# Kernel tuning notes

Hardware: AMD Instinct MI355X
Metric: run time of the kernel (lower is better)

## Reference

```python
import jax, jax.numpy as jnp
import numpy as np

B, S, E, FF = 8, 16384, 256, 1024
H, W, G = 128, 128, 16
Hn, Wn = H // G, W // G


def setup_inputs() -> dict:
    key = jax.random.key(0)
    ks = jax.random.split(key, 16)
    w = lambda k, shape: jax.random.normal(k, shape, jnp.float32) * 0.02
    return {
        "x": jax.random.normal(ks[0], (B, S, E), jnp.float32),
        "Wq": w(ks[1], (E, E)), "bq": jnp.zeros((E,), jnp.float32),
        "Wk": w(ks[2], (E, E)), "bk": jnp.zeros((E,), jnp.float32),
        "Wv": w(ks[3], (E, E)), "bv": jnp.zeros((E,), jnp.float32),
        "Wo": w(ks[4], (E, E)), "bo": jnp.zeros((E,), jnp.float32),
        "W1": w(ks[5], (E, FF)), "b1": jnp.zeros((FF,), jnp.float32),
        "W2": w(ks[6], (FF, E)), "b2": jnp.zeros((E,), jnp.float32),
        "g1": jnp.ones((E,), jnp.float32), "be1": jnp.zeros((E,), jnp.float32),
        "g2": jnp.ones((E,), jnp.float32), "be2": jnp.zeros((E,), jnp.float32),
    }


def _ln(x, g, b, eps=1e-5):
    m = jnp.mean(x, axis=-1, keepdims=True)
    v = jnp.mean(jnp.square(x - m), axis=-1, keepdims=True)
    return (x - m) * jax.lax.rsqrt(v + eps) * g + b


def _forward(x, Wq, bq, Wk, bk, Wv, bv, Wo, bo, W1, b1, W2, b2, g1, be1, g2, be2):
    # x: (B, S, E) -> (B, E, H, W), faithful to torch reshape (row-major reinterpret)
    x4 = x.reshape(B, E, H, W)
    # window partition: each window is the contiguous (E, G, G) block the torch loop slices
    xw = x4.reshape(B, E, Hn, G, Wn, G).transpose(0, 2, 4, 1, 3, 5)  # (B,Hn,Wn,E,G,G)
    # faithful raw reinterpretation (E,G,G) -> (G*G, E), matching grid.reshape(B,-1,E)
    t = xw.reshape(B, Hn * Wn, G * G, E)  # (B, nW, T=256, E)
    # single-head self-attention per window (batched over all windows at once)
    q = jnp.einsum('bwte,ef->bwtf', t, Wq) + bq
    k = jnp.einsum('bwte,ef->bwtf', t, Wk) + bk
    v = jnp.einsum('bwte,ef->bwtf', t, Wv) + bv
    scores = jnp.einsum('bwqe,bwke->bwqk', q, k) / jnp.sqrt(jnp.float32(E))
    attn = jax.nn.softmax(scores, axis=-1)
    o = jnp.einsum('bwqk,bwke->bwqe', attn, v)
    o = jnp.einsum('bwte,ef->bwtf', o, Wo) + bo  # (B, nW, 256, E)
    # reverse: view each window back to (E,G,G) and reassemble the feature map
    y = o.reshape(B, Hn, Wn, E, G, G).transpose(0, 3, 1, 4, 2, 5).reshape(B, E, H, W)
    y = y.reshape(B, S, E)  # faithful x.view(B, -1, E)
    # FFN (dropout is identity in eval) + residual with post-LN as written
    h = jax.nn.gelu(jnp.einsum('bse,ef->bsf', y, W1) + b1, approximate=False)
    ffn = jnp.einsum('bsf,fe->bse', h, W2) + b2
    y = y + _ln(ffn, g1, be1)
    y = y + _ln(y, g2, be2)
    return y


def reference(x, Wq, bq, Wk, bk, Wv, bv, Wo, bo, W1, b1, W2, b2, g1, be1, g2, be2):
    return _forward(x, Wq, bq, Wk, bk, Wv, bv, Wo, bo, W1, b1, W2, b2, g1, be1, g2, be2)
```

## Files before the change

### kernel.cpp

```cpp
#include <hip/hip_runtime.h>
#include <hip/hip_bf16.h>


typedef __bf16 bf16x8 __attribute__((ext_vector_type(8)));
typedef float  f32x4  __attribute__((ext_vector_type(4)));
typedef unsigned short us16;
typedef us16 us16x8 __attribute__((ext_vector_type(8)));
typedef us16 us16x4 __attribute__((ext_vector_type(4)));
typedef us16 us16x2 __attribute__((ext_vector_type(2)));

#define DI static __device__ __forceinline__

DI us16 f2b(float f){ __bf16 h = (__bf16)f; return __builtin_bit_cast(us16, h); }

DI bf16x8 cvt8(f32x4 a, f32x4 b){
  bf16x8 r;
  r[0]=(__bf16)a[0]; r[1]=(__bf16)a[1]; r[2]=(__bf16)a[2]; r[3]=(__bf16)a[3];
  r[4]=(__bf16)b[0]; r[5]=(__bf16)b[1]; r[6]=(__bf16)b[2]; r[7]=(__bf16)b[3];
  return r;
}
DI bf16x8 ld8(const us16* p){
  us16x8 v = *(const us16x8*)p;
  return __builtin_bit_cast(bf16x8, v);
}
DI f32x4 mfma16(bf16x8 a, bf16x8 b, f32x4 c){
  return __builtin_amdgcn_mfma_f32_16x16x32_bf16(a, b, c, 0, 0, 0);
}

DI bf16x8 ld_sw8(const char* base, int row, int f0){
  return ld8((const us16*)(base + row*512 + ((((f0>>3) ^ (row&7))) << 4)));
}
DI void st_sw1(char* base, int row, int f, us16 v){
  *(us16*)(base + row*512 + ((((f>>3) ^ (row&7))) << 4) + (f&7)*2) = v;
}
DI void st_sw4(char* base, int row, int f0, us16x4 v){
  *(us16x4*)(base + row*512 + ((((f0>>3) ^ (row&7))) << 4) + (f0&7)*2) = v;
}

DI bf16x8 ld_vt(const char* base, int row, int gg){
  return ld8((const us16*)(base + row*64 + (((gg ^ ((row>>1)&3))) << 4)));
}
DI void st_vt(char* base, int row, int col, us16 v){
  int c = col >> 3;
  *(us16*)(base + row*64 + (((c ^ ((row>>1)&3))) << 4) + (col&7)*2) = v;
}

__global__ void prep_w(const float* __restrict__ src, us16* __restrict__ dst,
                       int R, int C, int cshift){
  int idx = blockIdx.x*256 + threadIdx.x;
  if(idx >= R*C) return;
  int r = idx >> cshift;
  int c = idx & (C-1);
  dst[(size_t)c*R + r] = f2b(src[idx]);
}

__global__ __launch_bounds__(256, 2)
void kv_win(const float* __restrict__ x,
            const us16* __restrict__ WkT, const us16* __restrict__ WvT,
            const float* __restrict__ bk, const float* __restrict__ bv,
            char* __restrict__ KV)
{
  __shared__ __align__(16) char smem[65536];
  const int tid = threadIdx.x;
  const int wl = tid >> 6, lane = tid & 63, l15 = lane & 15, g = lane >> 4;
  const int blk = blockIdx.x;
  const int hw = blk & 1, tg = (blk>>1)&7, wh = (blk>>4)&7, b = blk>>7;
  const int win = wh*8 + hw*4 + wl;

  {
    const float* xb = x + (size_t)b*4194304 + (size_t)(tg*32)*16384 + wh*2048 + hw*64;
    const int prow = tid >> 4, pc = tid & 15;
    char* abase = smem + (pc>>2)*16384;
    const int f0 = prow*16 + (pc&3)*4;
    for(int t=0; t<32; t++){
      f32x4 v = *(const f32x4*)(xb + (size_t)t*16384 + prow*128 + pc*4);
      us16x4 pk; pk[0]=f2b(v[0]); pk[1]=f2b(v[1]); pk[2]=f2b(v[2]); pk[3]=f2b(v[3]);
      st_sw4(abase, t, f0, pk);
    }
  }
  __syncthreads();
  bf16x8 tA[2][8];
  #pragma unroll
  for(int mi=0; mi<2; mi++)
    #pragma unroll
    for(int kk=0; kk<8; kk++)
      tA[mi][kk] = ld_sw8(smem + wl*16384, mi*16 + l15, kk*32 + g*8);
  __syncthreads();

  char* outb = smem + wl*16384;
  const size_t wslot = (size_t)(b*64 + win);

  for(int n0=0; n0<16; n0++){
    f32x4 a0 = {0,0,0,0}, a1 = {0,0,0,0};
    const us16* wrow = WkT + (size_t)(n0*16 + l15)*256;
    #pragma unroll
    for(int kk=0; kk<8; kk++){
      bf16x8 wb = ld8(wrow + kk*32 + g*8);
      a0 = mfma16(tA[0][kk], wb, a0);
      a1 = mfma16(tA[1][kk], wb, a1);
    }
    float bias = bk[n0*16 + l15];
    #pragma unroll
    for(int r=0; r<4; r++){
      st_sw1(outb, g*4+r,    n0*16+l15, f2b(a0[r] + bias));
      st_sw1(outb, 16+g*4+r, n0*16+l15, f2b(a1[r] + bias));
    }
  }
  asm volatile("" ::: "memory");
  {
    char* dst = KV + wslot*262144 + tg*16384;
    #pragma unroll
    for(int i=0; i<16; i++)
      *(us16x8*)(dst + i*1024 + lane*16) = *(const us16x8*)(outb + i*1024 + lane*16);
  }
  asm volatile("" ::: "memory");

  for(int n0=0; n0<16; n0++){
    f32x4 a0 = {0,0,0,0}, a1 = {0,0,0,0};
    const us16* wrow = WvT + (size_t)(n0*16 + l15)*256;
    f32x4 bv4 = *(const f32x4*)(bv + n0*16 + g*4);
    #pragma unroll
    for(int kk=0; kk<8; kk++){
      bf16x8 wa = ld8(wrow + kk*32 + g*8);
      a0 = mfma16(wa, tA[0][kk], a0);
      a1 = mfma16(wa, tA[1][kk], a1);
    }
    #pragma unroll
    for(int r=0; r<4; r++){
      int jr = n0*16 + g*4 + r;
      st_vt(outb, jr, l15,      f2b(a0[r] + bv4[r]));
      st_vt(outb, jr, 16 + l15, f2b(a1[r] + bv4[r]));
    }
  }
  asm volatile("" ::: "memory");
  {
    char* dst = KV + wslot*262144 + 131072 + tg*16384;
    #pragma unroll
    for(int i=0; i<16; i++)
      *(us16x8*)(dst + i*1024 + lane*16) = *(const us16x8*)(outb + i*1024 + lane*16);
  }
}

DI void load_kv_regs(const char* slot, int kt, us16x8* r, int wid, int lane){
  const char* src = (wid < 4)
      ? slot + (size_t)kt*16384 + wid*4096
      : slot + 131072 + (size_t)kt*16384 + (wid-4)*4096;
  #pragma unroll
  for(int i=0; i<4; i++)
    r[i] = *(const us16x8*)(src + i*1024 + lane*16);
}
DI void write_kv_lds(char* kb, char* vb, const us16x8* r, int wid, int lane){
  char* dst = (wid < 4) ? kb + wid*4096 : vb + (wid-4)*4096;
  #pragma unroll
  for(int i=0; i<4; i++)
    *(us16x8*)(dst + i*1024 + lane*16) = r[i];
}

__global__ __launch_bounds__(512, 2)
void attn_hyb(const float* __restrict__ x,
              const us16* __restrict__ WqT, const float* __restrict__ bq,
              const char* __restrict__ KV,
              const us16* __restrict__ WoT, const float* __restrict__ bo,
              float* __restrict__ y)
{
  __shared__ __align__(16) char smem[135168];
  const int tid = threadIdx.x, wid = tid>>6, lane = tid&63, l15 = lane&15, g = lane>>4;
  const int blk = blockIdx.x;
  const int b   = blk >> 6;
  const int win = blk & 63;
  const size_t base = (size_t)b*4194304 + (size_t)(win>>3)*2048 + (size_t)(win&7)*16;
  const float* xb = x + base;
  float*       yb = y + base;
  const char*  slot = KV + (size_t)blk*262144;

  us16* Qw  = (us16*)(smem) + wid*(32*264);
  us16* Psw = (us16*)(smem + 65536) + wid*1280;
  const int r0 = wid*32;

  us16x8 stg[4];
  load_kv_regs(slot, 0, stg, wid, lane);

  bf16x8 tA[2][8];
  #pragma unroll
  for(int mi=0; mi<2; mi++){
    const float* trow = xb + (size_t)(r0 + mi*16 + l15)*16384;
    #pragma unroll
    for(int kk=0; kk<8; kk++){
      int f0 = kk*32 + g*8;
      const float* p = trow + (f0>>4)*128 + (f0&15);
      tA[mi][kk] = cvt8(*(const f32x4*)p, *(const f32x4*)(p+4));
    }
  }
  for(int n0=0; n0<16; n0++){
    f32x4 a0 = {0,0,0,0}, a1 = {0,0,0,0};
    const us16* wrow = WqT + (size_t)(n0*16 + l15)*256;
    #pragma unroll
    for(int kk=0; kk<8; kk++){
      bf16x8 wb = ld8(wrow + kk*32 + g*8);
      a0 = mfma16(tA[0][kk], wb, a0);
      a1 = mfma16(tA[1][kk], wb, a1);
    }
    float bias = bq[n0*16 + l15];
    #pragma unroll
    for(int r=0; r<4; r++){
      Qw[(g*4+r)*264      + n0*16 + l15] = f2b(a0[r] + bias);
      Qw[(16+g*4+r)*264   + n0*16 + l15] = f2b(a1[r] + bias);
    }
  }
  asm volatile("" ::: "memory");
  bf16x8 Qf[2][8];
  #pragma unroll
  for(int qn=0; qn<2; qn++)
    #pragma unroll
    for(int kk=0; kk<8; kk++)
      Qf[qn][kk] = ld8(Qw + (qn*16 + l15)*264 + kk*32 + g*8);
  __syncthreads();

  write_kv_lds(smem, smem + 32768, stg, wid, lane);

  float mr0 = -1e30f, mr1 = -1e30f, lr0 = 0.f, lr1 = 0.f;
  f32x4 Ot[16][2];
  const f32x4 zf = {0,0,0,0};
  #pragma unroll
  for(int i=0;i<16;i++){ Ot[i][0]=zf; Ot[i][1]=zf; }
  __syncthreads();

  for(int kt=0; kt<8; kt++){
    char* kb = (kt&1) ? smem + 16384 : smem;
    char* vb = (kt&1) ? smem + 49152 : smem + 32768;
    if(kt < 7) load_kv_regs(slot, kt+1, stg, wid, lane);
    f32x4 st[2][2] = {{zf,zf},{zf,zf}};
    #pragma unroll
    for(int kk=0; kk<8; kk++){
      int f0 = kk*32 + g*8;
      bf16x8 k0 = ld_sw8(kb, l15, f0);
      bf16x8 k1 = ld_sw8(kb, 16 + l15, f0);
      st[0][0] = mfma16(k0, Qf[0][kk], st[0][0]);
      st[0][1] = mfma16(k0, Qf[1][kk], st[0][1]);
      st[1][0] = mfma16(k1, Qf[0][kk], st[1][0]);
      st[1][1] = mfma16(k1, Qf[1][kk], st[1][1]);
    }
    #pragma unroll
    for(int mi=0; mi<2; mi++)
      #pragma unroll
      for(int qn=0; qn<2; qn++)
        #pragma unroll
        for(int r=0; r<4; r++) st[mi][qn][r] *= 0.0625f;
    float tm0 = st[0][0][0], tm1 = st[0][1][0];
    #pragma unroll
    for(int mi=0; mi<2; mi++)
      #pragma unroll
      for(int r=0; r<4; r++){
        tm0 = fmaxf(tm0, st[mi][0][r]);
        tm1 = fmaxf(tm1, st[mi][1][r]);
      }
    tm0 = fmaxf(tm0, __shfl_xor(tm0, 16)); tm0 = fmaxf(tm0, __shfl_xor(tm0, 32));
    tm1 = fmaxf(tm1, __shfl_xor(tm1, 16)); tm1 = fmaxf(tm1, __shfl_xor(tm1, 32));
    float mn0 = fmaxf(mr0, tm0), mn1 = fmaxf(mr1, tm1);
    float c0 = __expf(mr0 - mn0), c1 = __expf(mr1 - mn1);
    float ts0 = 0.f, ts1 = 0.f;
    #pragma unroll
    for(int mi=0; mi<2; mi++)
      #pragma unroll
      for(int r=0; r<4; r++){
        float p0 = __expf(st[mi][0][r] - mn0); st[mi][0][r] = p0; ts0 += p0;
        float p1 = __expf(st[mi][1][r] - mn1); st[mi][1][r] = p1; ts1 += p1;
      }
    ts0 += __shfl_xor(ts0, 16); ts0 += __shfl_xor(ts0, 32);
    ts1 += __shfl_xor(ts1, 16); ts1 += __shfl_xor(ts1, 32);
    lr0 = lr0*c0 + ts0;  lr1 = lr1*c1 + ts1;  mr0 = mn0;  mr1 = mn1;
    #pragma unroll
    for(int i=0;i<16;i++){
      #pragma unroll
      for(int r=0;r<4;r++){ Ot[i][0][r] *= c0; Ot[i][1][r] *= c1; }
    }
    #pragma unroll
    for(int qn=0; qn<2; qn++)
      #pragma unroll
      for(int mi=0; mi<2; mi++)
        #pragma unroll
        for(int rp=0; rp<2; rp++){
          us16x2 pk;
          pk[0] = f2b(st[mi][qn][rp*2]);
          pk[1] = f2b(st[mi][qn][rp*2+1]);
          *(us16x2*)((char*)Psw + (qn*16 + l15)*80 + (mi*16 + g*4 + rp*2)*2) = pk;
        }
    asm volatile("" ::: "memory");
    bf16x8 pb0 = ld8(Psw + l15*40 + g*8);
    bf16x8 pb1 = ld8(Psw + (16 + l15)*40 + g*8);
    #pragma unroll
    for(int fm=0; fm<16; fm++){
      bf16x8 va = ld_vt(vb, fm*16 + l15, g);
      Ot[fm][0] = mfma16(va, pb0, Ot[fm][0]);
      Ot[fm][1] = mfma16(va, pb1, Ot[fm][1]);
    }
    if(kt < 7){
      char* kbn = (kt&1) ? smem : smem + 16384;
      char* vbn = (kt&1) ? smem + 32768 : smem + 49152;
      write_kv_lds(kbn, vbn, stg, wid, lane);
    }
    __syncthreads();
  }

  float inv0 = 1.f/lr0, inv1 = 1.f/lr1;
  #pragma unroll
  for(int fm=0; fm<16; fm++)
    #pragma unroll
    for(int rp=0; rp<2; rp++){
      us16x2 p0, p1;
      p0[0]=f2b(Ot[fm][0][rp*2]*inv0);   p0[1]=f2b(Ot[fm][0][rp*2+1]*inv0);
      p1[0]=f2b(Ot[fm][1][rp*2]*inv1);   p1[1]=f2b(Ot[fm][1][rp*2+1]*inv1);
      *(us16x2*)((char*)Qw + l15*528      + (fm*16 + g*4 + rp*2)*2) = p0;
      *(us16x2*)((char*)Qw + (16+l15)*528 + (fm*16 + g*4 + rp*2)*2) = p1;
    }
  asm volatile("" ::: "memory");
  bf16x8 Of[2][8];
  #pragma unroll
  for(int qm=0; qm<2; qm++)
    #pragma unroll
    for(int kk=0; kk<8; kk++)
      Of[qm][kk] = ld8(Qw + (qm*16 + l15)*264 + kk*32 + g*8);
  for(int n0=0; n0<16; n0++){
    f32x4 a0 = {0,0,0,0}, a1 = {0,0,0,0};
    const us16* wrow = WoT + (size_t)(n0*16 + l15)*256;
    #pragma unroll
    for(int kk=0; kk<8; kk++){
      bf16x8 wb = ld8(wrow + kk*32 + g*8);
      a0 = mfma16(Of[0][kk], wb, a0);
      a1 = mfma16(Of[1][kk], wb, a1);
    }
    float bias = bo[n0*16 + l15];
    #pragma unroll
    for(int r=0; r<4; r++){
      yb[(size_t)(r0 + g*4 + r)*16384      + n0*128 + l15] = a0[r] + bias;
      yb[(size_t)(r0 + 16 + g*4 + r)*16384 + n0*128 + l15] = a1[r] + bias;
    }
  }
}

__global__ __launch_bounds__(512, 2)
void ffn_ln(float* y,
            const us16* __restrict__ W1T, const us16* __restrict__ W2T,
            const float* __restrict__ b1, const float* __restrict__ b2,
            const float* __restrict__ g1, const float* __restrict__ be1,
            const float* __restrict__ g2, const float* __restrict__ be2)
{
  __shared__ __align__(16) char smem[132096];
  us16*  h  = (us16*)smem;
  float* fl = (float*)smem;
  const int tid = threadIdx.x, wid = tid>>6, lane = tid&63, l15 = lane&15, g = lane>>4;
  float* Y = y + (size_t)blockIdx.x*64*256;

  bf16x8 ya[4][8];
  #pragma unroll
  for(int mi=0; mi<4; mi++){
    const float* p = Y + (size_t)(mi*16 + l15)*256;
    #pragma unroll
    for(int kk=0; kk<8; kk++){
      int f0 = kk*32 + g*8;
      ya[mi][kk] = cvt8(*(const f32x4*)(p + f0), *(const f32x4*)(p + f0 + 4));
    }
  }
  const f32x4 zf = {0,0,0,0};
  #pragma unroll 2
  for(int n0=0; n0<8; n0++){
    int j = wid*128 + n0*16 + l15;
    f32x4 acc[4] = {zf,zf,zf,zf};
    const us16* wrow = W1T + (size_t)j*256;
    #pragma unroll
    for(int kk=0; kk<8; kk++){
      bf16x8 wb = ld8(wrow + kk*32 + g*8);
      #pragma unroll
      for(int mi=0; mi<4; mi++) acc[mi] = mfma16(ya[mi][kk], wb, acc[mi]);
    }
    float bias = b1[j];
    #pragma unroll
    for(int mi=0; mi<4; mi++)
      #pragma unroll
      for(int r=0; r<4; r++){
        float v = acc[mi][r] + bias;
        v = 0.5f*v*(1.f + erff(v*0.70710678118654752f));
        h[(mi*16 + g*4 + r)*1032 + j] = f2b(v);
      }
  }
  __syncthreads();
  f32x4 acc2[4][2] = {{zf,zf},{zf,zf},{zf,zf},{zf,zf}};
  #pragma unroll 2
  for(int kk=0; kk<32; kk++){
    int f0 = kk*32 + g*8;
    bf16x8 ha[4];
    #pragma unroll
    for(int mi=0; mi<4; mi++) ha[mi] = ld8(h + (mi*16 + l15)*1032 + f0);
    #pragma unroll
    for(int n=0; n<2; n++){
      bf16x8 wb = ld8(W2T + (size_t)(wid*32 + n*16 + l15)*1024 + f0);
      #pragma unroll
      for(int mi=0; mi<4; mi++) acc2[mi][n] = mfma16(ha[mi], wb, acc2[mi][n]);
    }
  }
  __syncthreads();
  #pragma unroll
  for(int mi=0; mi<4; mi++)
    #pragma unroll
    for(int n=0; n<2; n++){
      float bias = b2[wid*32 + n*16 + l15];
      #pragma unroll
      for(int r=0; r<4; r++)
        fl[(mi*16 + g*4 + r)*260 + wid*32 + n*16 + l15] = acc2[mi][n][r] + bias;
    }
  __syncthreads();
  f32x4 G1  = *(const f32x4*)(g1  + lane*4);
  f32x4 BE1 = *(const f32x4*)(be1 + lane*4);
  f32x4 G2  = *(const f32x4*)(g2  + lane*4);
  f32x4 BE2 = *(const f32x4*)(be2 + lane*4);
  for(int rr=0; rr<8; rr++){
    int row = wid*8 + rr;
    f32x4 f  = *(const f32x4*)(fl + row*260 + lane*4);
    f32x4 yv = *(const f32x4*)(Y + (size_t)row*256 + lane*4);
    float s  = f[0]+f[1]+f[2]+f[3];
    float s2 = f[0]*f[0]+f[1]*f[1]+f[2]*f[2]+f[3]*f[3];
    #pragma unroll
    for(int m=1; m<=32; m<<=1){ s += __shfl_xor(s, m); s2 += __shfl_xor(s2, m); }
    float mu = s*(1.f/256.f);
    float rs = rsqrtf(fmaxf(s2*(1.f/256.f) - mu*mu, 0.f) + 1e-5f);
    f32x4 y1;
    #pragma unroll
    for(int i=0; i<4; i++) y1[i] = yv[i] + (f[i]-mu)*rs*G1[i] + BE1[i];
    float t1 = y1[0]+y1[1]+y1[2]+y1[3];
    float t2 = y1[0]*y1[0]+y1[1]*y1[1]+y1[2]*y1[2]+y1[3]*y1[3];
    #pragma unroll
    for(int m=1; m<=32; m<<=1){ t1 += __shfl_xor(t1, m); t2 += __shfl_xor(t2, m); }
    float mu2 = t1*(1.f/256.f);
    float rs2 = rsqrtf(fmaxf(t2*(1.f/256.f) - mu2*mu2, 0.f) + 1e-5f);
    f32x4 o;
    #pragma unroll
    for(int i=0; i<4; i++) o[i] = y1[i] + (y1[i]-mu2)*rs2*G2[i] + BE2[i];
    *(f32x4*)(Y + (size_t)row*256 + lane*4) = o;
  }
}

__global__ __launch_bounds__(512, 2)
void attn_win(const float* __restrict__ x,
              const us16* __restrict__ WqT, const us16* __restrict__ WkT,
              const us16* __restrict__ WvT, const us16* __restrict__ WoT,
              const float* __restrict__ bq, const float* __restrict__ bk,
              const float* __restrict__ bv, const float* __restrict__ bo,
              float* __restrict__ y)
{
  __shared__ __align__(16) char smem[135168];
  const int tid = threadIdx.x;
  const int wid = tid >> 6;
  const int lane = tid & 63;
  const int l15 = lane & 15;
  const int g = lane >> 4;

  const int blk = blockIdx.x;
  const int b   = blk >> 6;
  const int win = blk & 63;
  const size_t base = (size_t)b*4194304 + (size_t)(win>>3)*2048 + (size_t)(win&7)*16;
  const float* xb = x + base;
  float*       yb = y + base;

  us16* Qw    = (us16*)(smem) + wid*(32*264);
  char* slabb = smem;
  char* kldsb = smem + 16384;
  us16* Vt    = (us16*)(smem + 32768);
  us16* Psw   = (us16*)(smem + 53248) + wid*1280;

  const int r0 = wid*32;

  bf16x8 tA[2][8];
  #pragma unroll
  for(int mi=0; mi<2; mi++){
    const float* trow = xb + (size_t)(r0 + mi*16 + l15)*16384;
    #pragma unroll
    for(int kk=0; kk<8; kk++){
      int f0 = kk*32 + g*8;
      const float* p = trow + (f0>>4)*128 + (f0&15);
      tA[mi][kk] = cvt8(*(const f32x4*)p, *(const f32x4*)(p+4));
    }
  }
  for(int n0=0; n0<16; n0++){
    f32x4 a0 = {0,0,0,0}, a1 = {0,0,0,0};
    const us16* wrow = WqT + (size_t)(n0*16 + l15)*256;
    #pragma unroll
    for(int kk=0; kk<8; kk++){
      bf16x8 wb = ld8(wrow + kk*32 + g*8);
      a0 = mfma16(tA[0][kk], wb, a0);
      a1 = mfma16(tA[1][kk], wb, a1);
    }
    float bias = bq[n0*16 + l15];
    #pragma unroll
    for(int r=0; r<4; r++){
      Qw[(g*4+r)*264      + n0*16 + l15] = f2b(a0[r] + bias);
      Qw[(16+g*4+r)*264   + n0*16 + l15] = f2b(a1[r] + bias);
    }
  }
  asm volatile("" ::: "memory");
  bf16x8 Qf[2][8];
  #pragma unroll
  for(int qn=0; qn<2; qn++)
    #pragma unroll
    for(int kk=0; kk<8; kk++)
      Qf[qn][kk] = ld8(Qw + (qn*16 + l15)*264 + kk*32 + g*8);
  __syncthreads();

  const float bkv0 = bk[wid*32 + l15], bkv1 = bk[wid*32 + 16 + l15];
  float bvv[2][4];
  #pragma unroll
  for(int m=0; m<2; m++)
    #pragma unroll
    for(int r=0; r<4; r++)
      bvv[m][r] = bv[wid*32 + m*16 + g*4 + r];

  float mr0 = -1e30f, mr1 = -1e30f, lr0 = 0.f, lr1 = 0.f;
  f32x4 Ot[16][2];
  const f32x4 zf = {0,0,0,0};
  #pragma unroll
  for(int i=0;i<16;i++){ Ot[i][0]=zf; Ot[i][1]=zf; }

  for(int kt=0; kt<8; kt++){
    const int kr0 = kt*32;
    {
      int row = tid >> 4, c = tid & 15;
      const float* trow = xb + (size_t)(kr0 + row)*16384;
      #pragma unroll
      for(int j=0; j<4; j++){
        int f0 = (c + 16*j)*4;
        const float* p = trow + (f0>>4)*128 + (f0&15);
        f32x4 v = *(const f32x4*)p;
        us16x4 pk; pk[0]=f2b(v[0]); pk[1]=f2b(v[1]); pk[2]=f2b(v[2]); pk[3]=f2b(v[3]);
        st_sw4(slabb, row, f0, pk);
      }
    }
    __syncthreads();
    {
      f32x4 acc[2][2] = {{zf,zf},{zf,zf}};
      #pragma unroll
      for(int kk=0; kk<8; kk++){
        int f0 = kk*32 + g*8;
        bf16x8 a0 = ld_sw8(slabb, l15, f0);
        bf16x8 a1 = ld_sw8(slabb, 16 + l15, f0);
        #pragma unroll
        for(int n=0; n<2; n++){
          bf16x8 wb = ld8(WkT + (size_t)(wid*32 + n*16 + l15)*256 + f0);
          acc[n][0] = mfma16(a0, wb, acc[n][0]);
          acc[n][1] = mfma16(a1, wb, acc[n][1]);
        }
      }
      #pragma unroll
      for(int n=0; n<2; n++){
        float bias = n ? bkv1 : bkv0;
        #pragma unroll
        for(int r=0; r<4; r++){
          st_sw1(kldsb, g*4+r,      wid*32 + n*16 + l15, f2b(acc[n][0][r] + bias));
          st_sw1(kldsb, 16+g*4+r,   wid*32 + n*16 + l15, f2b(acc[n][1][r] + bias));
        }
      }
    }
    {
      f32x4 acc[2][2] = {{zf,zf},{zf,zf}};
      #pragma unroll
      for(int kk=0; kk<8; kk++){
        int f0 = kk*32 + g*8;
        bf16x8 b0 = ld_sw8(slabb, l15, f0);
        bf16x8 b1 = ld_sw8(slabb, 16 + l15, f0);
        #pragma unroll
        for(int fm=0; fm<2; fm++){
          bf16x8 wa = ld8(WvT + (size_t)(wid*32 + fm*16 + l15)*256 + f0);
          acc[fm][0] = mfma16(wa, b0, acc[fm][0]);
          acc[fm][1] = mfma16(wa, b1, acc[fm][1]);
        }
      }
      #pragma unroll
      for(int fm=0; fm<2; fm++)
        #pragma unroll
        for(int n=0; n<2; n++)
          #pragma unroll
          for(int r=0; r<4; r++){
            int f = wid*32 + fm*16 + g*4 + r;
            Vt[f*40 + n*16 + l15] = f2b(acc[fm][n][r] + bvv[fm][r]);
          }
    }
    __syncthreads();
    f32x4 st[2][2] = {{zf,zf},{zf,zf}};
    #pragma unroll
    for(int kk=0; kk<8; kk++){
      int f0 = kk*32 + g*8;
      bf16x8 k0 = ld_sw8(kldsb, l15, f0);
      bf16x8 k1 = ld_sw8(kldsb, 16 + l15, f0);
      st[0][0] = mfma16(k0, Qf[0][kk], st[0][0]);
      st[0][1] = mfma16(k0, Qf[1][kk], st[0][1]);
      st[1][0] = mfma16(k1, Qf[0][kk], st[1][0]);
      st[1][1] = mfma16(k1, Qf[1][kk], st[1][1]);
    }
    #pragma unroll
    for(int mi=0; mi<2; mi++)
      #pragma unroll
      for(int qn=0; qn<2; qn++)
        #pragma unroll
        for(int r=0; r<4; r++) st[mi][qn][r] *= 0.0625f;
    float tm0 = st[0][0][0], tm1 = st[0][1][0];
    #pragma unroll
    for(int mi=0; mi<2; mi++)
      #pragma unroll
      for(int r=0; r<4; r++){
        tm0 = fmaxf(tm0, st[mi][0][r]);
        tm1 = fmaxf(tm1, st[mi][1][r]);
      }
    tm0 = fmaxf(tm0, __shfl_xor(tm0, 16)); tm0 = fmaxf(tm0, __shfl_xor(tm0, 32));
    tm1 = fmaxf(tm1, __shfl_xor(tm1, 16)); tm1 = fmaxf(tm1, __shfl_xor(tm1, 32));
    float mn0 = fmaxf(mr0, tm0), mn1 = fmaxf(mr1, tm1);
    float c0 = __expf(mr0 - mn0), c1 = __expf(mr1 - mn1);
    float ts0 = 0.f, ts1 = 0.f;
    #pragma unroll
    for(int mi=0; mi<2; mi++)
      #pragma unroll
      for(int r=0; r<4; r++){
        float p0 = __expf(st[mi][0][r] - mn0); st[mi][0][r] = p0; ts0 += p0;
        float p1 = __expf(st[mi][1][r] - mn1); st[mi][1][r] = p1; ts1 += p1;
      }
    ts0 += __shfl_xor(ts0, 16); ts0 += __shfl_xor(ts0, 32);
    ts1 += __shfl_xor(ts1, 16); ts1 += __shfl_xor(ts1, 32);
    lr0 = lr0*c0 + ts0;  lr1 = lr1*c1 + ts1;  mr0 = mn0;  mr1 = mn1;
    #pragma unroll
    for(int i=0;i<16;i++){
      #pragma unroll
      for(int r=0;r<4;r++){ Ot[i][0][r] *= c0; Ot[i][1][r] *= c1; }
    }
    #pragma unroll
    for(int qn=0; qn<2; qn++)
      #pragma unroll
      for(int mi=0; mi<2; mi++)
        #pragma unroll
        for(int rp=0; rp<2; rp++){
          us16x2 pk;
          pk[0] = f2b(st[mi][qn][rp*2]);
          pk[1] = f2b(st[mi][qn][rp*2+1]);
          *(us16x2*)((char*)Psw + (qn*16 + l15)*80 + (mi*16 + g*4 + rp*2)*2) = pk;
        }
    asm volatile("" ::: "memory");
    bf16x8 pb0 = ld8(Psw + l15*40 + g*8);
    bf16x8 pb1 = ld8(Psw + (16 + l15)*40 + g*8);
    #pragma unroll
    for(int fm=0; fm<16; fm++){
      bf16x8 va = ld8(Vt + (fm*16 + l15)*40 + g*8);
      Ot[fm][0] = mfma16(va, pb0, Ot[fm][0]);
      Ot[fm][1] = mfma16(va, pb1, Ot[fm][1]);
    }
    __syncthreads();
  }

  float inv0 = 1.f/lr0, inv1 = 1.f/lr1;
  #pragma unroll
  for(int fm=0; fm<16; fm++)
    #pragma unroll
    for(int rp=0; rp<2; rp++){
      us16x2 p0, p1;
      p0[0]=f2b(Ot[fm][0][rp*2]*inv0);   p0[1]=f2b(Ot[fm][0][rp*2+1]*inv0);
      p1[0]=f2b(Ot[fm][1][rp*2]*inv1);   p1[1]=f2b(Ot[fm][1][rp*2+1]*inv1);
      *(us16x2*)((char*)Qw + l15*528      + (fm*16 + g*4 + rp*2)*2) = p0;
      *(us16x2*)((char*)Qw + (16+l15)*528 + (fm*16 + g*4 + rp*2)*2) = p1;
    }
  asm volatile("" ::: "memory");
  bf16x8 Of[2][8];
  #pragma unroll
  for(int qm=0; qm<2; qm++)
    #pragma unroll
    for(int kk=0; kk<8; kk++)
      Of[qm][kk] = ld8(Qw + (qm*16 + l15)*264 + kk*32 + g*8);
  for(int n0=0; n0<16; n0++){
    f32x4 a0 = {0,0,0,0}, a1 = {0,0,0,0};
    const us16* wrow = WoT + (size_t)(n0*16 + l15)*256;
    #pragma unroll
    for(int kk=0; kk<8; kk++){
      bf16x8 wb = ld8(wrow + kk*32 + g*8);
      a0 = mfma16(Of[0][kk], wb, a0);
      a1 = mfma16(Of[1][kk], wb, a1);
    }
    float bias = bo[n0*16 + l15];
    #pragma unroll
    for(int r=0; r<4; r++){
      yb[(size_t)(r0 + g*4 + r)*16384      + n0*128 + l15] = a0[r] + bias;
      yb[(size_t)(r0 + 16 + g*4 + r)*16384 + n0*128 + l15] = a1[r] + bias;
    }
  }
}

extern "C" void kernel_launch(void* const* d_in, const int* in_sizes, int n_in,
                              void* d_out, int out_size, void* d_ws, size_t ws_size,
                              hipStream_t stream)
{
  const float* x   = (const float*)d_in[0];
  const float* Wq  = (const float*)d_in[1];
  const float* bq  = (const float*)d_in[2];
  const float* Wk  = (const float*)d_in[3];
  const float* bk  = (const float*)d_in[4];
  const float* Wv  = (const float*)d_in[5];
  const float* bv  = (const float*)d_in[6];
  const float* Wo  = (const float*)d_in[7];
  const float* bo  = (const float*)d_in[8];
  const float* W1  = (const float*)d_in[9];
  const float* b1  = (const float*)d_in[10];
  const float* W2  = (const float*)d_in[11];
  const float* b2  = (const float*)d_in[12];
  const float* g1  = (const float*)d_in[13];
  const float* be1 = (const float*)d_in[14];
  const float* g2  = (const float*)d_in[15];
  const float* be2 = (const float*)d_in[16];
  float* out = (float*)d_out;
  char* ws = (char*)d_ws;

  const size_t KVBYTES = 134217728ull;
  const size_t NEED    = KVBYTES + 1572864ull;

  if(ws_size >= NEED){
    char* wbase = ws + KVBYTES;
    us16* WqT = (us16*)(wbase);
    us16* WkT = (us16*)(wbase + 131072);
    us16* WvT = (us16*)(wbase + 262144);
    us16* WoT = (us16*)(wbase + 393216);
    us16* W1T = (us16*)(wbase + 524288);
    us16* W2T = (us16*)(wbase + 1048576);

    prep_w<<<dim3(256),  dim3(256), 0, stream>>>(Wq, WqT, 256, 256, 8);
    prep_w<<<dim3(256),  dim3(256), 0, stream>>>(Wk, WkT, 256, 256, 8);
    prep_w<<<dim3(256),  dim3(256), 0, stream>>>(Wv, WvT, 256, 256, 8);
    prep_w<<<dim3(256),  dim3(256), 0, stream>>>(Wo, WoT, 256, 256, 8);
    prep_w<<<dim3(1024), dim3(256), 0, stream>>>(W1, W1T, 256, 1024, 10);
    prep_w<<<dim3(1024), dim3(256), 0, stream>>>(W2, W2T, 1024, 256, 8);

    kv_win<<<dim3(1024), dim3(256), 0, stream>>>(x, WkT, WvT, bk, bv, ws);
    attn_hyb<<<dim3(512), dim3(512), 0, stream>>>(x, WqT, bq, ws, WoT, bo, out);
    ffn_ln<<<dim3(2048), dim3(512), 0, stream>>>(out, W1T, W2T, b1, b2,
                                                 g1, be1, g2, be2);
  } else {
    us16* WqT = (us16*)(ws);
    us16* WkT = (us16*)(ws + 131072);
    us16* WvT = (us16*)(ws + 262144);
    us16* WoT = (us16*)(ws + 393216);
    us16* W1T = (us16*)(ws + 524288);
    us16* W2T = (us16*)(ws + 1048576);

    prep_w<<<dim3(256),  dim3(256), 0, stream>>>(Wq, WqT, 256, 256, 8);
    prep_w<<<dim3(256),  dim3(256), 0, stream>>>(Wk, WkT, 256, 256, 8);
    prep_w<<<dim3(256),  dim3(256), 0, stream>>>(Wv, WvT, 256, 256, 8);
    prep_w<<<dim3(256),  dim3(256), 0, stream>>>(Wo, WoT, 256, 256, 8);
    prep_w<<<dim3(1024), dim3(256), 0, stream>>>(W1, W1T, 256, 1024, 10);
    prep_w<<<dim3(1024), dim3(256), 0, stream>>>(W2, W2T, 1024, 256, 8);

    attn_win<<<dim3(512), dim3(512), 0, stream>>>(x, WqT, WkT, WvT, WoT,
                                                  bq, bk, bv, bo, out);
    ffn_ln<<<dim3(2048), dim3(512), 0, stream>>>(out, W1T, W2T, b1, b2,
                                                 g1, be1, g2, be2);
  }
}
```

Before: 850.3 us.

## Move Q projection into the K/V projection kernel and stage Q in workspace

The Q projection now runs inside the window K/V projection kernel, reusing the staged bf16 input tile, and writes a swizzled bf16 Q image to a new 64MB workspace region. A new attention kernel loads Q fragments straight from that image instead of re-reading fp32 x and running the Q GEMM itself. The shared attention loop is factored into a helper. This removes the second fp32 read of x and the Q GEMM from the attention kernel, at the cost of an extra 64MB bf16 write and read. It also needs a larger workspace and falls back to the old path otherwise.

```diff
diff --git a/kernel.cpp b/kernel.cpp
--- a/kernel.cpp
+++ b/kernel.cpp
@@ -52,6 +52,121 @@
   int r = idx >> cshift;
   int c = idx & (C-1);
   dst[(size_t)c*R + r] = f2b(src[idx]);
+}
+
+__global__ __launch_bounds__(256, 2)
+void qkv_win(const float* __restrict__ x,
+             const us16* __restrict__ WqT, const us16* __restrict__ WkT,
+             const us16* __restrict__ WvT,
+             const float* __restrict__ bq, const float* __restrict__ bk,
+             const float* __restrict__ bv,
+             char* __restrict__ Qimg,
+             char* __restrict__ KV)
+{
+  __shared__ __align__(16) char smem[65536];
+  const int tid = threadIdx.x;
+  const int wl = tid >> 6, lane = tid & 63, l15 = lane & 15, g = lane >> 4;
+  const int blk = blockIdx.x;
+  const int hw = blk & 1, tg = (blk>>1)&7, wh = (blk>>4)&7, b = blk>>7;
+  const int win = wh*8 + hw*4 + wl;
+
+  {
+    const float* xb = x + (size_t)b*4194304 + (size_t)(tg*32)*16384 + wh*2048 + hw*64;
+    const int prow = tid >> 4, pc = tid & 15;
+    char* abase = smem + (pc>>2)*16384;
+    const int f0 = prow*16 + (pc&3)*4;
+    for(int t=0; t<32; t++){
+      f32x4 v = *(const f32x4*)(xb + (size_t)t*16384 + prow*128 + pc*4);
+      us16x4 pk; pk[0]=f2b(v[0]); pk[1]=f2b(v[1]); pk[2]=f2b(v[2]); pk[3]=f2b(v[3]);
+      st_sw4(abase, t, f0, pk);
+    }
+  }
+  __syncthreads();
+  bf16x8 tA[2][8];
+  #pragma unroll
+  for(int mi=0; mi<2; mi++)
+    #pragma unroll
+    for(int kk=0; kk<8; kk++)
+      tA[mi][kk] = ld_sw8(smem + wl*16384, mi*16 + l15, kk*32 + g*8);
+  __syncthreads();
+
+  char* outb = smem + wl*16384;
+  const size_t wslot = (size_t)(b*64 + win);
+
+  for(int n0=0; n0<16; n0++){
+    f32x4 a0 = {0,0,0,0}, a1 = {0,0,0,0};
+    const us16* wrow = WqT + (size_t)(n0*16 + l15)*256;
+    #pragma unroll
+    for(int kk=0; kk<8; kk++){
+      bf16x8 wb = ld8(wrow + kk*32 + g*8);
+      a0 = mfma16(tA[0][kk], wb, a0);
+      a1 = mfma16(tA[1][kk], wb, a1);
+    }
+    float bias = bq[n0*16 + l15];
+    #pragma unroll
+    for(int r=0; r<4; r++){
+      st_sw1(outb, g*4+r,    n0*16+l15, f2b(a0[r] + bias));
+      st_sw1(outb, 16+g*4+r, n0*16+l15, f2b(a1[r] + bias));
+    }
+  }
+  asm volatile("" ::: "memory");
+  {
+    char* dst = Qimg + (wslot*8 + tg)*16384;
+    #pragma unroll
+    for(int i=0; i<16; i++)
+      *(us16x8*)(dst + i*1024 + lane*16) = *(const us16x8*)(outb + i*1024 + lane*16);
+  }
+  asm volatile("" ::: "memory");
+
+  for(int n0=0; n0<16; n0++){
+    f32x4 a0 = {0,0,0,0}, a1 = {0,0,0,0};
+    const us16* wrow = WkT + (size_t)(n0*16 + l15)*256;
+    #pragma unroll
+    for(int kk=0; kk<8; kk++){
+      bf16x8 wb = ld8(wrow + kk*32 + g*8);
+      a0 = mfma16(tA[0][kk], wb, a0);
+      a1 = mfma16(tA[1][kk], wb, a1);
+    }
+    float bias = bk[n0*16 + l15];
+    #pragma unroll
+    for(int r=0; r<4; r++){
+      st_sw1(outb, g*4+r,    n0*16+l15, f2b(a0[r] + bias));
+      st_sw1(outb, 16+g*4+r, n0*16+l15, f2b(a1[r] + bias));
+    }
+  }
+  asm volatile("" ::: "memory");
+  {
+    char* dst = KV + wslot*262144 + tg*16384;
+    #pragma unroll
+    for(int i=0; i<16; i++)
+      *(us16x8*)(dst + i*1024 + lane*16) = *(const us16x8*)(outb + i*1024 + lane*16);
+  }
+  asm volatile("" ::: "memory");
+
+  for(int n0=0; n0<16; n0++){
+    f32x4 a0 = {0,0,0,0}, a1 = {0,0,0,0};
+    const us16* wrow = WvT + (size_t)(n0*16 + l15)*256;
+    f32x4 bv4 = *(const f32x4*)(bv + n0*16 + g*4);
+    #pragma unroll
+    for(int kk=0; kk<8; kk++){
+      bf16x8 wa = ld8(wrow + kk*32 + g*8);
+      a0 = mfma16(wa, tA[0][kk], a0);
+      a1 = mfma16(wa, tA[1][kk], a1);
+    }
+    #pragma unroll
+    for(int r=0; r<4; r++){
+      int jr = n0*16 + g*4 + r;
+      st_vt(outb, jr, l15,      f2b(a0[r] + bv4[r]));
+      st_vt(outb, jr, 16 + l15, f2b(a1[r] + bv4[r]));
+    }
+  }
+  asm volatile("" ::: "memory");
+  {
+    char* dst = KV + wslot*262144 + 131072 + tg*16384;
+    #pragma unroll
+    for(int i=0; i<16; i++)
+      *(us16x8*)(dst + i*1024 + lane*16) = *(const us16x8*)(outb + i*1024 + lane*16);
+  }
 }
 
 __global__ __launch_bounds__(256, 2)
@@ -154,6 +269,165 @@
   #pragma unroll
   for(int i=0; i<4; i++)
     *(us16x8*)(dst + i*1024 + lane*16) = r[i];
+}
+
+DI void attn_core_loop(char* smem, us16* Psw, const char* slot,
+                       const bf16x8 Qf[2][8], us16x8* stg,
+                       const us16* WoT, const float* bo, float* yb,
+                       int wid, int lane, int l15, int g, int r0)
+{
+  us16* Qw = (us16*)(smem) + wid*(32*264);
+  float mr0 = -1e30f, mr1 = -1e30f, lr0 = 0.f, lr1 = 0.f;
+  f32x4 Ot[16][2];
+  const f32x4 zf = {0,0,0,0};
+  #pragma unroll
+  for(int i=0;i<16;i++){ Ot[i][0]=zf; Ot[i][1]=zf; }
+  __syncthreads();
+
+  for(int kt=0; kt<8; kt++){
+    char* kb = (kt&1) ? smem + 16384 : smem;
+    char* vb = (kt&1) ? smem + 49152 : smem + 32768;
+    if(kt < 7) load_kv_regs(slot, kt+1, stg, wid, lane);
+    f32x4 st[2][2] = {{zf,zf},{zf,zf}};
+    #pragma unroll
+    for(int kk=0; kk<8; kk++){
+      int f0 = kk*32 + g*8;
+      bf16x8 k0 = ld_sw8(kb, l15, f0);
+      bf16x8 k1 = ld_sw8(kb, 16 + l15, f0);
+      st[0][0] = mfma16(k0, Qf[0][kk], st[0][0]);
+      st[0][1] = mfma16(k0, Qf[1][kk], st[0][1]);
+      st[1][0] = mfma16(k1, Qf[0][kk], st[1][0]);
+      st[1][1] = mfma16(k1, Qf[1][kk], st[1][1]);
+    }
+    #pragma unroll
+    for(int mi=0; mi<2; mi++)
+      #pragma unroll
+      for(int qn=0; qn<2; qn++)
+        #pragma unroll
+        for(int r=0; r<4; r++) st[mi][qn][r] *= 0.0625f;
+    float tm0 = st[0][0][0], tm1 = st[0][1][0];
+    #pragma unroll
+    for(int mi=0; mi<2; mi++)
+      #pragma unroll
+      for(int r=0; r<4; r++){
+        tm0 = fmaxf(tm0, st[mi][0][r]);
+        tm1 = fmaxf(tm1, st[mi][1][r]);
+      }
+    tm0 = fmaxf(tm0, __shfl_xor(tm0, 16)); tm0 = fmaxf(tm0, __shfl_xor(tm0, 32));
+    tm1 = fmaxf(tm1, __shfl_xor(tm1, 16)); tm1 = fmaxf(tm1, __shfl_xor(tm1, 32));
+    float mn0 = fmaxf(mr0, tm0), mn1 = fmaxf(mr1, tm1);
+    float c0 = __expf(mr0 - mn0), c1 = __expf(mr1 - mn1);
+    float ts0 = 0.f, ts1 = 0.f;
+    #pragma unroll
+    for(int mi=0; mi<2; mi++)
+      #pragma unroll
+      for(int r=0; r<4; r++){
+        float p0 = __expf(st[mi][0][r] - mn0); st[mi][0][r] = p0; ts0 += p0;
+        float p1 = __expf(st[mi][1][r] - mn1); st[mi][1][r] = p1; ts1 += p1;
+      }
+    ts0 += __shfl_xor(ts0, 16); ts0 += __shfl_xor(ts0, 32);
+    ts1 += __shfl_xor(ts1, 16); ts1 += __shfl_xor(ts1, 32);
+    lr0 = lr0*c0 + ts0;  lr1 = lr1*c1 + ts1;  mr0 = mn0;  mr1 = mn1;
+    #pragma unroll
+    for(int i=0;i<16;i++){
+      #pragma unroll
+      for(int r=0;r<4;r++){ Ot[i][0][r] *= c0; Ot[i][1][r] *= c1; }
+    }
+    #pragma unroll
+    for(int qn=0; qn<2; qn++)
+      #pragma unroll
+      for(int mi=0; mi<2; mi++)
+        #pragma unroll
+        for(int rp=0; rp<2; rp++){
+          us16x2 pk;
+          pk[0] = f2b(st[mi][qn][rp*2]);
+          pk[1] = f2b(st[mi][qn][rp*2+1]);
+          *(us16x2*)((char*)Psw + (qn*16 + l15)*80 + (mi*16 + g*4 + rp*2)*2) = pk;
+        }
+    asm volatile("" ::: "memory");
+    bf16x8 pb0 = ld8(Psw + l15*40 + g*8);
+    bf16x8 pb1 = ld8(Psw + (16 + l15)*40 + g*8);
+    #pragma unroll
+    for(int fm=0; fm<16; fm++){
+      bf16x8 va = ld_vt(vb, fm*16 + l15, g);
+      Ot[fm][0] = mfma16(va, pb0, Ot[fm][0]);
+      Ot[fm][1] = mfma16(va, pb1, Ot[fm][1]);
+    }
+    if(kt < 7){
+      char* kbn = (kt&1) ? smem : smem + 16384;
+      char* vbn = (kt&1) ? smem + 32768 : smem + 49152;
+      write_kv_lds(kbn, vbn, stg, wid, lane);
+    }
+    __syncthreads();
+  }
+
+  float inv0 = 1.f/lr0, inv1 = 1.f/lr1;
+  #pragma unroll
+  for(int fm=0; fm<16; fm++)
+    #pragma unroll
+    for(int rp=0; rp<2; rp++){
+      us16x2 p0, p1;
+      p0[0]=f2b(Ot[fm][0][rp*2]*inv0);   p0[1]=f2b(Ot[fm][0][rp*2+1]*inv0);
+      p1[0]=f2b(Ot[fm][1][rp*2]*inv1);   p1[1]=f2b(Ot[fm][1][rp*2+1]*inv1);
+      *(us16x2*)((char*)Qw + l15*528      + (fm*16 + g*4 + rp*2)*2) = p0;
+      *(us16x2*)((char*)Qw + (16+l15)*528 + (fm*16 + g*4 + rp*2)*2) = p1;
+    }
+  asm volatile("" ::: "memory");
+  bf16x8 Of[2][8];
+  #pragma unroll
+  for(int qm=0; qm<2; qm++)
+    #pragma unroll
+    for(int kk=0; kk<8; kk++)
+      Of[qm][kk] = ld8(Qw + (qm*16 + l15)*264 + kk*32 + g*8);
+  for(int n0=0; n0<16; n0++){
+    f32x4 a0 = {0,0,0,0}, a1 = {0,0,0,0};
+    const us16* wrow = WoT + (size_t)(n0*16 + l15)*256;
+    #pragma unroll
+    for(int kk=0; kk<8; kk++){
+      bf16x8 wb = ld8(wrow + kk*32 + g*8);
+      a0 = mfma16(Of[0][kk], wb, a0);
+      a1 = mfma16(Of[1][kk], wb, a1);
+    }
+    float bias = bo[n0*16 + l15];
+    #pragma unroll
+    for(int r=0; r<4; r++){
+      yb[(size_t)(r0 + g*4 + r)*16384      + n0*128 + l15] = a0[r] + bias;
+      yb[(size_t)(r0 + 16 + g*4 + r)*16384 + n0*128 + l15] = a1[r] + bias;
+    }
+  }
+}
+
+__global__ __launch_bounds__(512, 2)
+void attn_hyb2(const char* __restrict__ Qimg, const char* __restrict__ KV,
+               const us16* __restrict__ WoT, const float* __restrict__ bo,
+               float* __restrict__ y)
+{
+  __shared__ __align__(16) char smem[135168];
+  const int tid = threadIdx.x, wid = tid>>6, lane = tid&63, l15 = lane&15, g = lane>>4;
+  const int blk = blockIdx.x;
+  const int b   = blk >> 6;
+  const int win = blk & 63;
+  const size_t base = (size_t)b*4194304 + (size_t)(win>>3)*2048 + (size_t)(win&7)*16;
+  float*       yb = y + base;
+  const char*  slot = KV + (size_t)blk*262144;
+  const char*  Qt = Qimg + ((size_t)blk*8 + wid)*16384;
+  us16* Psw = (us16*)(smem + 65536) + wid*1280;
+  const int r0 = wid*32;
+
+  us16x8 stg[4];
+  load_kv_regs(slot, 0, stg, wid, lane);
+
+  bf16x8 Qf[2][8];
+  #pragma unroll
+  for(int qn=0; qn<2; qn++)
+    #pragma unroll
+    for(int kk=0; kk<8; kk++){
+      int row = qn*16 + l15;
+      Qf[qn][kk] = ld8((const us16*)(Qt + row*512 + ((((kk*4+g) ^ (l15&7))) << 4)));
+    }
+
+  write_kv_lds(smem, smem + 32768, stg, wid, lane);
+  attn_core_loop(smem, Psw, slot, Qf, stg, WoT, bo, yb, wid, lane, l15, g, r0);
 }
 
 __global__ __launch_bounds__(512, 2)
@@ -217,125 +491,7 @@
   __syncthreads();
 
   write_kv_lds(smem, smem + 32768, stg, wid, lane);
-
-  float mr0 = -1e30f, mr1 = -1e30f, lr0 = 0.f, lr1 = 0.f;
-  f32x4 Ot[16][2];
-  const f32x4 zf = {0,0,0,0};
-  #pragma unroll
-  for(int i=0;i<16;i++){ Ot[i][0]=zf; Ot[i][1]=zf; }
-  __syncthreads();
-
-  for(int kt=0; kt<8; kt++){
-    char* kb = (kt&1) ? smem + 16384 : smem;
-    char* vb = (kt&1) ? smem + 49152 : smem + 32768;
-    if(kt < 7) load_kv_regs(slot, kt+1, stg, wid, lane);
-    f32x4 st[2][2] = {{zf,zf},{zf,zf}};
-    #pragma unroll
-    for(int kk=0; kk<8; kk++){
-      int f0 = kk*32 + g*8;
-      bf16x8 k0 = ld_sw8(kb, l15, f0);
-      bf16x8 k1 = ld_sw8(kb, 16 + l15, f0);
-      st[0][0] = mfma16(k0, Qf[0][kk], st[0][0]);
-      st[0][1] = mfma16(k0, Qf[1][kk], st[0][1]);
-      st[1][0] = mfma16(k1, Qf[0][kk], st[1][0]);
-      st[1][1] = mfma16(k1, Qf[1][kk], st[1][1]);
-    }
-    #pragma unroll
-    for(int mi=0; mi<2; mi++)
-      #pragma unroll
-      for(int qn=0; qn<2; qn++)
-        #pragma unroll
-        for(int r=0; r<4; r++) st[mi][qn][r] *= 0.0625f;
-    float tm0 = st[0][0][0], tm1 = st[0][1][0];
-    #pragma unroll
-    for(int mi=0; mi<2; mi++)
-      #pragma unroll
-      for(int r=0; r<4; r++){
-        tm0 = fmaxf(tm0, st[mi][0][r]);
-        tm1 = fmaxf(tm1, st[mi][1][r]);
-      }
-    tm0 = fmaxf(tm0, __shfl_xor(tm0, 16)); tm0 = fmaxf(tm0, __shfl_xor(tm0, 32));
-    tm1 = fmaxf(tm1, __shfl_xor(tm1, 16)); tm1 = fmaxf(tm1, __shfl_xor(tm1, 32));
-    float mn0 = fmaxf(mr0, tm0), mn1 = fmaxf(mr1, tm1);
-    float c0 = __expf(mr0 - mn0), c1 = __expf(mr1 - mn1);
-    float ts0 = 0.f, ts1 = 0.f;
-    #pragma unroll
-    for(int mi=0; mi<2; mi++)
-      #pragma unroll
-      for(int r=0; r<4; r++){
-        float p0 = __expf(st[mi][0][r] - mn0); st[mi][0][r] = p0; ts0 += p0;
-        float p1 = __expf(st[mi][1][r] - mn1); st[mi][1][r] = p1; ts1 += p1;
-      }
-    ts0 += __shfl_xor(ts0, 16); ts0 += __shfl_xor(ts0, 32);
-    ts1 += __shfl_xor(ts1, 16); ts1 += __shfl_xor(ts1, 32);
-    lr0 = lr0*c0 + ts0;  lr1 = lr1*c1 + ts1;  mr0 = mn0;  mr1 = mn1;
-    #pragma unroll
-    for(int i=0;i<16;i++){
-      #pragma unroll
-      for(int r=0;r<4;r++){ Ot[i][0][r] *= c0; Ot[i][1][r] *= c1; }
-    }
-    #pragma unroll
-    for(int qn=0; qn<2; qn++)
-      #pragma unroll
-      for(int mi=0; mi<2; mi++)
-        #pragma unroll
-        for(int rp=0; rp<2; rp++){
-          us16x2 pk;
-          pk[0] = f2b(st[mi][qn][rp*2]);
-          pk[1] = f2b(st[mi][qn][rp*2+1]);
-          *(us16x2*)((char*)Psw + (qn*16 + l15)*80 + (mi*16 + g*4 + rp*2)*2) = pk;
-        }
-    asm volatile("" ::: "memory");
-    bf16x8 pb0 = ld8(Psw + l15*40 + g*8);
-    bf16x8 pb1 = ld8(Psw + (16 + l15)*40 + g*8);
-    #pragma unroll
-    for(int fm=0; fm<16; fm++){
-      bf16x8 va = ld_vt(vb, fm*16 + l15, g);
-      Ot[fm][0] = mfma16(va, pb0, Ot[fm][0]);
-      Ot[fm][1] = mfma16(va, pb1, Ot[fm][1]);
-    }
-    if(kt < 7){
-      char* kbn = (kt&1) ? smem : smem + 16384;
-      char* vbn = (kt&1) ? smem + 32768 : smem + 49152;
-      write_kv_lds(kbn, vbn, stg, wid, lane);
-    }
-    __syncthreads();
-  }
-
-  float inv0 = 1.f/lr0, inv1 = 1.f/lr1;
-  #pragma unroll
-  for(int fm=0; fm<16; fm++)
-    #pragma unroll
-    for(int rp=0; rp<2; rp++){
-      us16x2 p0, p1;
-      p0[0]=f2b(Ot[fm][0][rp*2]*inv0);   p0[1]=f2b(Ot[fm][0][rp*2+1]*inv0);
-      p1[0]=f2b(Ot[fm][1][rp*2]*inv1);   p1[1]=f2b(Ot[fm][1][rp*2+1]*inv1);
-      *(us16x2*)((char*)Qw + l15*528      + (fm*16 + g*4 + rp*2)*2) = p0;
-      *(us16x2*)((char*)Qw + (16+l15)*528 + (fm*16 + g*4 + rp*2)*2) = p1;
-    }
-  asm volatile("" ::: "memory");
-  bf16x8 Of[2][8];
-  #pragma unroll
-  for(int qm=0; qm<2; qm++)
-    #pragma unroll
-    for(int kk=0; kk<8; kk++)
-      Of[qm][kk] = ld8(Qw + (qm*16 + l15)*264 + kk*32 + g*8);
-  for(int n0=0; n0<16; n0++){
-    f32x4 a0 = {0,0,0,0}, a1 = {0,0,0,0};
-    const us16* wrow = WoT + (size_t)(n0*16 + l15)*256;
-    #pragma unroll
-    for(int kk=0; kk<8; kk++){
-      bf16x8 wb = ld8(wrow + kk*32 + g*8);
-      a0 = mfma16(Of[0][kk], wb, a0);
-      a1 = mfma16(Of[1][kk], wb, a1);
-    }
-    float bias = bo[n0*16 + l15];
-    #pragma unroll
-    for(int r=0; r<4; r++){
-      yb[(size_t)(r0 + g*4 + r)*16384      + n0*128 + l15] = a0[r] + bias;
-      yb[(size_t)(r0 + 16 + g*4 + r)*16384 + n0*128 + l15] = a1[r] + bias;
-    }
-  }
+  attn_core_loop(smem, Psw, slot, Qf, stg, WoT, bo, yb, wid, lane, l15, g, r0);
 }
 
 __global__ __launch_bounds__(512, 2)
@@ -712,9 +868,33 @@
   char* ws = (char*)d_ws;
 
   const size_t KVBYTES = 134217728ull;
-  const size_t NEED    = KVBYTES + 1572864ull;
-
-  if(ws_size >= NEED){
+  const size_t QBYTES  = 67108864ull;
+  const size_t NEED_B  = KVBYTES + 1572864ull;
+  const size_t NEED_A  = KVBYTES + QBYTES + 1572864ull;
+
+  if(ws_size >= NEED_A){
+    char* Qimg  = ws + KVBYTES;
+    char* wbase = ws + KVBYTES + QBYTES;
+    us16* WqT = (us16*)(wbase);
+    us16* WkT = (us16*)(wbase + 131072);
+    us16* WvT = (us16*)(wbase + 262144);
+    us16* WoT = (us16*)(wbase + 393216);
+    us16* W1T = (us16*)(wbase + 524288);
+    us16* W2T = (us16*)(wbase + 1048576);
+
+    prep_w<<<dim3(256),  dim3(256), 0, stream>>>(Wq, WqT, 256, 256, 8);
+    prep_w<<<dim3(256),  dim3(256), 0, stream>>>(Wk, WkT, 256, 256, 8);
+    prep_w<<<dim3(256),  dim3(256), 0, stream>>>(Wv, WvT, 256, 256, 8);
+    prep_w<<<dim3(256),  dim3(256), 0, stream>>>(Wo, WoT, 256, 256, 8);
+    prep_w<<<dim3(1024), dim3(256), 0, stream>>>(W1, W1T, 256, 1024, 10);
+    prep_w<<<dim3(1024), dim3(256), 0, stream>>>(W2, W2T, 1024, 256, 8);
+
+    qkv_win<<<dim3(1024), dim3(256), 0, stream>>>(x, WqT, WkT, WvT, bq, bk, bv,
+                                                  Qimg, ws);
+    attn_hyb2<<<dim3(512), dim3(512), 0, stream>>>(Qimg, ws, WoT, bo, out);
+    ffn_ln<<<dim3(2048), dim3(512), 0, stream>>>(out, W1T, W2T, b1, b2,
+                                                 g1, be1, g2, be2);
+  } else if(ws_size >= NEED_B){
     char* wbase = ws + KVBYTES;
     us16* WqT = (us16*)(wbase);
     us16* WkT = (us16*)(wbase + 131072);
```

Result: faster. 825.4 us (-2.9%).
